# Kernel tuning notes

Hardware: AMD Instinct MI355X
Metric: run time of the kernel (lower is better)

Reference implementation:

```python
import jax, jax.numpy as jnp
import numpy as np

N_Q = 10000
B, S = 128, 200
M = 50          # memory_size
DK = 64         # memory_key_state_dim == q_embed_dim == final_fc_dim
DV = 128        # memory_value_state_dim == qa_embed_dim
F = 64          # final_fc_dim


def setup_inputs() -> dict:
    key = jax.random.key(0)
    ks = jax.random.split(key, 14)
    q_data = jax.random.randint(ks[0], (B, S), 0, N_Q + 1)
    qa_data = jax.random.randint(ks[1], (B, S), 0, 2 * N_Q + 1)
    # target in {-1 (pad), 0, 1}
    target = jax.random.randint(ks[2], (B, S), -1, 2).astype(jnp.float32)
    q_embed_w = jax.random.normal(ks[3], (N_Q + 1, DK), jnp.float32) * 0.1
    q_embed_w = q_embed_w.at[0].set(0.0)  # padding_idx=0
    qa_embed_w = jax.random.normal(ks[4], (2 * N_Q + 1, DV), jnp.float32) * 0.1
    qa_embed_w = qa_embed_w.at[0].set(0.0)
    mem_key = jax.random.normal(ks[5], (M, DK), jnp.float32) * (2.0 / DK) ** 0.5
    init_mem_value = jax.random.normal(ks[6], (M, DV), jnp.float32) * (2.0 / DV) ** 0.5
    erase_w = jax.random.normal(ks[7], (DV, DV), jnp.float32) * (2.0 / DV) ** 0.5
    erase_b = jnp.zeros((DV,), jnp.float32)
    add_w = jax.random.normal(ks[8], (DV, DV), jnp.float32) * (2.0 / DV) ** 0.5
    add_b = jnp.zeros((DV,), jnp.float32)
    read_w = jax.random.normal(ks[9], (F, DV + F), jnp.float32) * (2.0 / (DV + F)) ** 0.5
    read_b = jnp.zeros((F,), jnp.float32)
    pred_w = jax.random.normal(ks[10], (1, F), jnp.float32) * (2.0 / F) ** 0.5
    pred_b = jnp.zeros((1,), jnp.float32)
    return {
        'q_data': q_data, 'qa_data': qa_data, 'target': target,
        'q_embed_w': q_embed_w, 'qa_embed_w': qa_embed_w,
        'mem_key': mem_key, 'init_mem_value': init_mem_value,
        'erase_w': erase_w, 'erase_b': erase_b,
        'add_w': add_w, 'add_b': add_b,
        'read_w': read_w, 'read_b': read_b,
        'pred_w': pred_w, 'pred_b': pred_b,
    }


def reference(q_data, qa_data, target, q_embed_w, qa_embed_w, mem_key,
              init_mem_value, erase_w, erase_b, add_w, add_b,
              read_w, read_b, pred_w, pred_b):
    q_e = q_embed_w[q_data]    # [B,S,DK]
    qa_e = qa_embed_w[qa_data]  # [B,S,DV]
    Mv0 = jnp.broadcast_to(init_mem_value, (q_data.shape[0],) + init_mem_value.shape)  # [B,M,DV]

    def step(Mv, x):
        q, qa = x                                           # [B,DK], [B,DV]
        w = jax.nn.softmax(q @ mem_key.T, axis=1)           # addressing -> [B,M]
        read = jnp.einsum('bm,bmv->bv', w, Mv)              # weighted read (before write)
        e = jax.nn.sigmoid(qa @ erase_w.T + erase_b)        # [B,DV]
        a = jnp.tanh(qa @ add_w.T + add_b)                  # [B,DV]
        Mv_new = Mv * (1.0 - w[:, :, None] * e[:, None, :]) + w[:, :, None] * a[:, None, :]
        return Mv_new, read

    _, reads = jax.lax.scan(step, Mv0, (q_e.transpose(1, 0, 2), qa_e.transpose(1, 0, 2)))
    reads = reads.transpose(1, 0, 2)                        # [B,S,DV]

    h = jnp.tanh(jnp.concatenate([reads, q_e], axis=-1) @ read_w.T + read_b)  # [B,S,F]
    logits = (h @ pred_w.T + pred_b)[..., 0]                # [B,S]

    mask = target >= 0
    t = jnp.where(mask, target, 0.0)
    # stable BCE with logits
    bce = jnp.maximum(logits, 0.0) - logits * t + jnp.log1p(jnp.exp(-jnp.abs(logits)))
    n_valid = jnp.maximum(jnp.sum(mask.astype(jnp.float32)), 1.0)
    loss = jnp.sum(jnp.where(mask, bce, 0.0)) / n_valid
    probs = jnp.where(mask, jax.nn.sigmoid(logits), 0.0)    # masked predictions, fixed shape
    return loss, probs
```

## Files before the change

### kernel.cpp

```cpp
#include <hip/hip_runtime.h>
#include <math.h>

#define BB 128
#define SS 200
#define MM 50
#define DKK 64
#define DVV 128
#define FF 64
#define NROW (BB*SS)

#define WROW 64
#define NFCB (NROW/64)
#define WLDS 136
#define FLDS 200
#define CLEN 25
#define MP 25
#define NSCB 100

#define W_OFF   0L
#define EA_OFF  (W_OFF + (long)NROW*WROW)
#define R_OFF   (EA_OFF + (long)NROW*DVV*2)
#define ACC_OFF (R_OFF + (long)NROW*DVV)

typedef __attribute__((ext_vector_type(8))) short bf16x8;
typedef __attribute__((ext_vector_type(4))) float f32x4;
typedef __attribute__((ext_vector_type(2))) float f32x2;

__device__ __forceinline__ float rlane(float v, int l) {
    return __builtin_bit_cast(float, __builtin_amdgcn_readlane(__builtin_bit_cast(unsigned, v), l));
}
__device__ __forceinline__ short f2bf(float f) {
    unsigned u = __builtin_bit_cast(unsigned, f);
    u += 0x7fff + ((u >> 16) & 1);
    return (short)(u >> 16);
}
__device__ __forceinline__ bf16x8 cvt8(const float* p) {
    float4 lo = *(const float4*)p;
    float4 hi = *(const float4*)(p + 4);
    bf16x8 f;
    f[0] = f2bf(lo.x); f[1] = f2bf(lo.y); f[2] = f2bf(lo.z); f[3] = f2bf(lo.w);
    f[4] = f2bf(hi.x); f[5] = f2bf(hi.y); f[6] = f2bf(hi.z); f[7] = f2bf(hi.w);
    return f;
}

__global__ __launch_bounds__(256) void k_pre(const int* __restrict__ q_data,
                                             const float* __restrict__ q_embed_w,
                                             const float* __restrict__ mem_key,
                                             const int* __restrict__ qa_data,
                                             const float* __restrict__ qa_embed_w,
                                             const float* __restrict__ erase_w,
                                             const float* __restrict__ erase_b,
                                             const float* __restrict__ add_w,
                                             const float* __restrict__ add_b,
                                             float* __restrict__ w_out,
                                             float* __restrict__ EA,
                                             float* __restrict__ acc) {
    __shared__ union {
        short  wl[2 * 128 * WLDS];
        float4 mk[MM * 16];
    } sh;
    int tid = threadIdx.x;
    int bid = blockIdx.x;

    if (bid < NSCB) {
        if (bid == 0 && tid == 0) {
            acc[0] = 0.f; acc[1] = 0.f;
            ((unsigned*)acc)[2] = 0u;
        }
        const float4* mkg = (const float4*)mem_key;
        for (int i = tid; i < MM * 16; i += 256) sh.mk[i] = mkg[i];
        __syncthreads();

        int item = bid * 256 + tid;
        int qidx = q_data[item];
        const float4* qg = (const float4*)(q_embed_w + (long)qidx * DKK);
        float4 q[16];
#pragma unroll
        for (int i = 0; i < 16; i++) q[i] = qg[i];

        float s[MM];
        float mx = -1e30f;
#pragma unroll 2
        for (int m = 0; m < MM; m++) {
            float a = 0.f;
#pragma unroll
            for (int k4 = 0; k4 < 16; k4++) {
                float4 mkv = sh.mk[m * 16 + k4];
                float4 qv = q[k4];
                a = fmaf(qv.x, mkv.x, a);
                a = fmaf(qv.y, mkv.y, a);
                a = fmaf(qv.z, mkv.z, a);
                a = fmaf(qv.w, mkv.w, a);
            }
            s[m] = a;
            mx = fmaxf(mx, a);
        }
        float sum = 0.f;
#pragma unroll
        for (int m = 0; m < MM; m++) { s[m] = expf(s[m] - mx); sum += s[m]; }
        float inv = 1.f / sum;

        float* wo = w_out + (long)item * WROW;
#pragma unroll
        for (int m = 0; m < MM; m++) wo[m] = s[m] * inv;
#pragma unroll
        for (int m = MM; m < WROW; m++) wo[m] = 0.f;
        return;
    }

    int r0 = (bid - NSCB) * 64;
    int lane = tid & 63;
    int wv = tid >> 6;
    int n = lane & 15;
    int quad = lane >> 4;

    for (int i = tid; i < 8192; i += 256) {
        int mat = i >> 12;
        int r = (i >> 5) & 127;
        int p = i & 31;
        float4 src = *(const float4*)((mat ? add_w : erase_w) + r * 128 + p * 4);
        short4 d;
        d.x = f2bf(src.x); d.y = f2bf(src.y); d.z = f2bf(src.z); d.w = f2bf(src.w);
        *(short4*)(sh.wl + (mat * 128 + r) * WLDS + p * 4) = d;
    }

    int arow = r0 + wv * 16 + n;
    int qidx = qa_data[arow];
    const float* qp = qa_embed_w + (long)qidx * DVV + quad * 8;
    bf16x8 afrag[4];
#pragma unroll
    for (int kb = 0; kb < 4; kb++) afrag[kb] = cvt8(qp + kb * 32);

    float eb_[8], ab_[8];
#pragma unroll
    for (int vt = 0; vt < 8; vt++) {
        eb_[vt] = erase_b[vt * 16 + n];
        ab_[vt] = add_b[vt * 16 + n];
    }
    __syncthreads();

    int rowbase = r0 + wv * 16 + quad * 4;
#pragma unroll 2
    for (int vt = 0; vt < 8; vt++) {
        int vrow = vt * 16 + n;
        f32x4 ae = {0.f, 0.f, 0.f, 0.f};
        f32x4 aa = {0.f, 0.f, 0.f, 0.f};
#pragma unroll
        for (int kb = 0; kb < 4; kb++) {
            bf16x8 be = *(const bf16x8*)(sh.wl + vrow * WLDS + kb * 32 + quad * 8);
            bf16x8 ba = *(const bf16x8*)(sh.wl + (128 + vrow) * WLDS + kb * 32 + quad * 8);
            ae = __builtin_amdgcn_mfma_f32_16x16x32_bf16(afrag[kb], be, ae, 0, 0, 0);
            aa = __builtin_amdgcn_mfma_f32_16x16x32_bf16(afrag[kb], ba, aa, 0, 0, 0);
        }
        int v = vt * 16 + n;
        float eb = eb_[vt], ab = ab_[vt];
#pragma unroll
        for (int r = 0; r < 4; r++) {
            float ev = 1.f / (1.f + __expf(-(ae[r] + eb)));
            float av = 2.f / (1.f + __expf(-2.f * (aa[r] + ab))) - 1.f;
            float2 o; o.x = ev; o.y = av;
            *(float2*)(EA + (((long)(rowbase + r)) * DVV + v) * 2) = o;
        }
    }
}

__global__ __launch_bounds__(512, 2) void k_scan(const float* __restrict__ w_pad,
                                                 const float* __restrict__ EA,
                                                 const float* __restrict__ init_mv,
                                                 float* __restrict__ R) {
    __shared__ float Sb[MM * 64];
    int b   = blockIdx.x >> 1;
    int vh  = blockIdx.x & 1;
    int tid = threadIdx.x;
    int lane  = tid & 63;
    int chunk = tid >> 6;
    int v  = vh * 64 + lane;
    int t0 = chunk * CLEN;

    const float* wbase = w_pad + ((long)b * SS + t0) * WROW;
    const float* eab   = EA + (((long)b * SS + t0) * DVV + v) * 2;
    float*       Rb    = R + ((long)b * SS + t0) * DVV + v;

    const f32x2 one = {1.f, 1.f};

    f32x2 A2[MP], B2[MP];
#pragma unroll
    for (int j = 0; j < MP; j++) { A2[j] = one; B2[j] = (f32x2){0.f, 0.f}; }

    float  w_cur  = wbase[lane];
    float2 ea_cur = *(const float2*)eab;
#pragma unroll 1
    for (int t = 0; t < CLEN; t++) {
        int tp = (t + 1 < CLEN) ? t + 1 : t;
        float  w_nxt  = wbase[tp * WROW + lane];
        float2 ea_nxt = *(const float2*)(eab + (long)tp * DVV * 2);
        f32x2 e2 = {ea_cur.x, ea_cur.x};
        f32x2 a2 = {ea_cur.y, ea_cur.y};
#pragma unroll
        for (int j = 0; j < MP; j++) {
            f32x2 w2 = {rlane(w_cur, 2 * j), rlane(w_cur, 2 * j + 1)};
            f32x2 alpha = one - w2 * e2;
            A2[j] = A2[j] * alpha;
            B2[j] = alpha * B2[j] + w2 * a2;
        }
        w_cur = w_nxt; ea_cur = ea_nxt;
    }

    f32x2 Mv[MP];
    if (chunk == 0) {
#pragma unroll
        for (int j = 0; j < MP; j++) {
            Mv[j].x = init_mv[(2 * j) * DVV + v];
            Mv[j].y = init_mv[(2 * j + 1) * DVV + v];
        }
#pragma unroll
        for (int j = 0; j < MP; j++) {
            f32x2 nb = A2[j] * Mv[j] + B2[j];
            Sb[(2 * j) * 64 + lane] = nb.x;
            Sb[(2 * j + 1) * 64 + lane] = nb.y;
        }
    }
    __syncthreads();
    for (int c = 1; c < 8; c++) {
        if (chunk == c) {
#pragma unroll
            for (int j = 0; j < MP; j++) {
                Mv[j].x = Sb[(2 * j) * 64 + lane];
                Mv[j].y = Sb[(2 * j + 1) * 64 + lane];
            }
            if (c < 7) {
#pragma unroll
                for (int j = 0; j < MP; j++) {
                    f32x2 nb = A2[j] * Mv[j] + B2[j];
                    Sb[(2 * j) * 64 + lane] = nb.x;
                    Sb[(2 * j + 1) * 64 + lane] = nb.y;
                }
            }
        }
        __syncthreads();
    }

    w_cur  = wbase[lane];
    ea_cur = *(const float2*)eab;
#pragma unroll 1
    for (int t = 0; t < CLEN; t++) {
        int tp = (t + 1 < CLEN) ? t + 1 : t;
        float  w_nxt  = wbase[tp * WROW + lane];
        float2 ea_nxt = *(const float2*)(eab + (long)tp * DVV * 2);
        f32x2 e2 = {ea_cur.x, ea_cur.x};
        f32x2 a2 = {ea_cur.y, ea_cur.y};
        f32x2 rd2 = {0.f, 0.f};
#pragma unroll
        for (int j = 0; j < MP; j++) {
            f32x2 w2 = {rlane(w_cur, 2 * j), rlane(w_cur, 2 * j + 1)};
            rd2 = rd2 + w2 * Mv[j];
            f32x2 alpha = one - w2 * e2;
            Mv[j] = alpha * Mv[j] + w2 * a2;
        }
        Rb[t * DVV] = rd2.x + rd2.y;
        w_cur = w_nxt; ea_cur = ea_nxt;
    }
}

__global__ __launch_bounds__(256) void k_fc(const float* __restrict__ Rr,
                                            const int* __restrict__ q_data,
                                            const float* __restrict__ q_embed_w,
                                            const float* __restrict__ read_w,
                                            const float* __restrict__ read_b,
                                            const float* __restrict__ pred_w,
                                            const float* __restrict__ pred_b,
                                            const float* __restrict__ target,
                                            float* __restrict__ out,
                                            float* __restrict__ acc) {
    __shared__ short Wl[64 * FLDS];
    __shared__ float2 red[4];
    int tid = threadIdx.x;
    int r0 = blockIdx.x * 64;
    int lane = tid & 63;
    int wv = tid >> 6;
    int n = lane & 15;
    int quad = lane >> 4;

    for (int i = tid; i < 3072; i += 256) {
        int f = i / 48, p = i - f * 48;
        float4 src = *(const float4*)(read_w + f * 192 + p * 4);
        short4 d;
        d.x = f2bf(src.x); d.y = f2bf(src.y); d.z = f2bf(src.z); d.w = f2bf(src.w);
        *(short4*)(Wl + f * FLDS + p * 4) = d;
    }

    int arow = r0 + wv * 16 + n;
    const float* rp = Rr + (long)arow * DVV + quad * 8;
    int qi = q_data[arow];
    const float* qp = q_embed_w + (long)qi * DKK + quad * 8;
    bf16x8 afrag[6];
#pragma unroll
    for (int kb = 0; kb < 4; kb++) afrag[kb] = cvt8(rp + kb * 32);
#pragma unroll
    for (int kb = 0; kb < 2; kb++) afrag[4 + kb] = cvt8(qp + kb * 32);

    float rb_[4], pw_[4];
#pragma unroll
    for (int ft = 0; ft < 4; ft++) {
        rb_[ft] = read_b[ft * 16 + n];
        pw_[ft] = pred_w[ft * 16 + n];
    }
    float pb = pred_b[0];
    __syncthreads();

    int rowbase = r0 + wv * 16 + quad * 4;
    float pv[4] = {0.f, 0.f, 0.f, 0.f};
#pragma unroll
    for (int ft = 0; ft < 4; ft++) {
        int f = ft * 16 + n;
        f32x4 ac = {0.f, 0.f, 0.f, 0.f};
#pragma unroll
        for (int kb = 0; kb < 6; kb++) {
            bf16x8 bfr = *(const bf16x8*)(Wl + f * FLDS + kb * 32 + quad * 8);
            ac = __builtin_amdgcn_mfma_f32_16x16x32_bf16(afrag[kb], bfr, ac, 0, 0, 0);
        }
        float rb = rb_[ft], pw = pw_[ft];
#pragma unroll
        for (int r = 0; r < 4; r++) {
            float h = 2.f / (1.f + __expf(-2.f * (ac[r] + rb))) - 1.f;
            pv[r] = fmaf(pw, h, pv[r]);
        }
    }

    float bce_sum = 0.f, cnt = 0.f;
#pragma unroll
    for (int r = 0; r < 4; r++) {
        float p = pv[r];
        p += __shfl_xor(p, 1, 64);
        p += __shfl_xor(p, 2, 64);
        p += __shfl_xor(p, 4, 64);
        p += __shfl_xor(p, 8, 64);
        if (n == 0) {
            int row = rowbase + r;
            float tgt = target[row];
            float logit = p + pb;
            float prob = 0.f;
            if (tgt >= 0.f) {
                prob = 1.f / (1.f + __expf(-logit));
                float bce = fmaxf(logit, 0.f) - logit * tgt + log1pf(__expf(-fabsf(logit)));
                bce_sum += bce;
                cnt += 1.f;
            }
            out[1 + row] = prob;
        }
    }
    bce_sum += __shfl_xor(bce_sum, 16, 64);
    bce_sum += __shfl_xor(bce_sum, 32, 64);
    cnt     += __shfl_xor(cnt, 16, 64);
    cnt     += __shfl_xor(cnt, 32, 64);
    if (lane == 0) { red[wv].x = bce_sum; red[wv].y = cnt; }
    __syncthreads();
    if (tid == 0) {
        float bsum = red[0].x + red[1].x + red[2].x + red[3].x;
        float csum = red[0].y + red[1].y + red[2].y + red[3].y;
        atomicAdd(&acc[0], bsum);
        atomicAdd(&acc[1], csum);
        __threadfence();
        unsigned prev = atomicAdd((unsigned*)acc + 2, 1u);
        if (prev == NFCB - 1) {
            __threadfence();
            float B = atomicAdd(&acc[0], 0.f);
            float C = atomicAdd(&acc[1], 0.f);
            out[0] = B / fmaxf(C, 1.f);
        }
    }
}

extern "C" void kernel_launch(void* const* d_in, const int* in_sizes, int n_in,
                              void* d_out, int out_size, void* d_ws, size_t ws_size,
                              hipStream_t stream) {
    const int*   q_data     = (const int*)d_in[0];
    const int*   qa_data    = (const int*)d_in[1];
    const float* target     = (const float*)d_in[2];
    const float* q_embed_w  = (const float*)d_in[3];
    const float* qa_embed_w = (const float*)d_in[4];
    const float* mem_key    = (const float*)d_in[5];
    const float* init_mv    = (const float*)d_in[6];
    const float* erase_w    = (const float*)d_in[7];
    const float* erase_b    = (const float*)d_in[8];
    const float* add_w      = (const float*)d_in[9];
    const float* add_b      = (const float*)d_in[10];
    const float* read_w     = (const float*)d_in[11];
    const float* read_b     = (const float*)d_in[12];
    const float* pred_w     = (const float*)d_in[13];
    const float* pred_b     = (const float*)d_in[14];
    float* out = (float*)d_out;
    float* ws  = (float*)d_ws;

    float* w_all = ws + W_OFF;
    float* EA    = ws + EA_OFF;
    float* R     = ws + R_OFF;
    float* acc   = ws + ACC_OFF;

    k_pre<<<NSCB + NROW / 64, 256, 0, stream>>>(q_data, q_embed_w, mem_key,
                                                qa_data, qa_embed_w,
                                                erase_w, erase_b, add_w, add_b,
                                                w_all, EA, acc);
    k_scan<<<BB * 2, 512, 0, stream>>>(w_all, EA, init_mv, R);
    k_fc<<<NFCB, 256, 0, stream>>>(R, q_data, q_embed_w, read_w, read_b,
                                   pred_w, pred_b, target, out, acc);
}
```

Measured before the change: 182.2 us.

## Split scan memory slots across two blocks and sum partial reads in FC

The recurrent scan kernel now splits the 50 memory slots into two halves handled by separate blocks, doubling the grid to 512 blocks and halving the serial per-thread work and register state. Each half writes its own partial read vector, and the FC kernel adds the two partials before converting to bf16. This trades extra global writes and reads of a second read buffer for more parallelism on the latency-bound scan. Padded slots beyond 50 rely on zero addressing weights in the padded w buffer.

```diff
diff --git a/kernel.cpp b/kernel.cpp
--- a/kernel.cpp
+++ b/kernel.cpp
@@ -14,13 +14,14 @@
 #define WLDS 136
 #define FLDS 200
 #define CLEN 25
-#define MP 25
+#define MPH 13
 #define NSCB 100
 
 #define W_OFF   0L
 #define EA_OFF  (W_OFF + (long)NROW*WROW)
 #define R_OFF   (EA_OFF + (long)NROW*DVV*2)
-#define ACC_OFF (R_OFF + (long)NROW*DVV)
+#define RP1_OFF (R_OFF + (long)NROW*DVV)
+#define ACC_OFF (RP1_OFF + (long)NROW*DVV)
 
 typedef __attribute__((ext_vector_type(8))) short bf16x8;
 typedef __attribute__((ext_vector_type(4))) float f32x4;
@@ -40,6 +41,16 @@
     bf16x8 f;
     f[0] = f2bf(lo.x); f[1] = f2bf(lo.y); f[2] = f2bf(lo.z); f[3] = f2bf(lo.w);
     f[4] = f2bf(hi.x); f[5] = f2bf(hi.y); f[6] = f2bf(hi.z); f[7] = f2bf(hi.w);
+    return f;
+}
+__device__ __forceinline__ bf16x8 cvt8sum(const float* p, const float* q) {
+    float4 alo = *(const float4*)p, ahi = *(const float4*)(p + 4);
+    float4 blo = *(const float4*)q, bhi = *(const float4*)(q + 4);
+    bf16x8 f;
+    f[0] = f2bf(alo.x + blo.x); f[1] = f2bf(alo.y + blo.y);
+    f[2] = f2bf(alo.z + blo.z); f[3] = f2bf(alo.w + blo.w);
+    f[4] = f2bf(ahi.x + bhi.x); f[5] = f2bf(ahi.y + bhi.y);
+    f[6] = f2bf(ahi.z + bhi.z); f[7] = f2bf(ahi.w + bhi.w);
     return f;
 }
 
@@ -167,25 +178,31 @@
 __global__ __launch_bounds__(512, 2) void k_scan(const float* __restrict__ w_pad,
                                                  const float* __restrict__ EA,
                                                  const float* __restrict__ init_mv,
-                                                 float* __restrict__ R) {
-    __shared__ float Sb[MM * 64];
-    int b   = blockIdx.x >> 1;
-    int vh  = blockIdx.x & 1;
+                                                 float* __restrict__ Rp0,
+                                                 float* __restrict__ Rp1) {
+    __shared__ float Sb[52 * 64];
+    int bid = blockIdx.x;
+    int mh  = bid & 1;
+    int vh  = (bid >> 1) & 1;
+    int b   = bid >> 2;
     int tid = threadIdx.x;
     int lane  = tid & 63;
     int chunk = tid >> 6;
     int v  = vh * 64 + lane;
     int t0 = chunk * CLEN;
+    int j0 = mh * MPH;
+    int l0 = 2 * j0;
+    int sb0 = l0 * 64 + lane;
 
     const float* wbase = w_pad + ((long)b * SS + t0) * WROW;
     const float* eab   = EA + (((long)b * SS + t0) * DVV + v) * 2;
-    float*       Rb    = R + ((long)b * SS + t0) * DVV + v;
+    float*       Rb    = (mh ? Rp1 : Rp0) + ((long)b * SS + t0) * DVV + v;
 
     const f32x2 one = {1.f, 1.f};
 
-    f32x2 A2[MP], B2[MP];
-#pragma unroll
-    for (int j = 0; j < MP; j++) { A2[j] = one; B2[j] = (f32x2){0.f, 0.f}; }
+    f32x2 A2[MPH], B2[MPH];
+#pragma unroll
+    for (int j = 0; j < MPH; j++) { A2[j] = one; B2[j] = (f32x2){0.f, 0.f}; }
 
     float  w_cur  = wbase[lane];
     float2 ea_cur = *(const float2*)eab;
@@ -197,8 +214,8 @@
         f32x2 e2 = {ea_cur.x, ea_cur.x};
         f32x2 a2 = {ea_cur.y, ea_cur.y};
 #pragma unroll
-        for (int j = 0; j < MP; j++) {
-            f32x2 w2 = {rlane(w_cur, 2 * j), rlane(w_cur, 2 * j + 1)};
+        for (int j = 0; j < MPH; j++) {
+            f32x2 w2 = {rlane(w_cur, l0 + 2 * j), rlane(w_cur, l0 + 2 * j + 1)};
             f32x2 alpha = one - w2 * e2;
             A2[j] = A2[j] * alpha;
             B2[j] = alpha * B2[j] + w2 * a2;
@@ -206,34 +223,37 @@
         w_cur = w_nxt; ea_cur = ea_nxt;
     }
 
-    f32x2 Mv[MP];
+    f32x2 Mv[MPH];
     if (chunk == 0) {
 #pragma unroll
-        for (int j = 0; j < MP; j++) {
-            Mv[j].x = init_mv[(2 * j) * DVV + v];
-            Mv[j].y = init_mv[(2 * j + 1) * DVV + v];
-        }
-#pragma unroll
-        for (int j = 0; j < MP; j++) {
+        for (int j = 0; j < MPH; j++) {
+            int m0 = l0 + 2 * j, m1 = m0 + 1;
+            if (m0 > MM - 2) m0 = MM - 2;
+            if (m1 > MM - 1) m1 = MM - 1;
+            Mv[j].x = init_mv[m0 * DVV + v];
+            Mv[j].y = init_mv[m1 * DVV + v];
+        }
+#pragma unroll
+        for (int j = 0; j < MPH; j++) {
             f32x2 nb = A2[j] * Mv[j] + B2[j];
-            Sb[(2 * j) * 64 + lane] = nb.x;
-            Sb[(2 * j + 1) * 64 + lane] = nb.y;
+            Sb[sb0 + (2 * j) * 64] = nb.x;
+            Sb[sb0 + (2 * j + 1) * 64] = nb.y;
         }
     }
     __syncthreads();
     for (int c = 1; c < 8; c++) {
         if (chunk == c) {
 #pragma unroll
-            for (int j = 0; j < MP; j++) {
-                Mv[j].x = Sb[(2 * j) * 64 + lane];
-                Mv[j].y = Sb[(2 * j + 1) * 64 + lane];
+            for (int j = 0; j < MPH; j++) {
+                Mv[j].x = Sb[sb0 + (2 * j) * 64];
+                Mv[j].y = Sb[sb0 + (2 * j + 1) * 64];
             }
             if (c < 7) {
 #pragma unroll
-                for (int j = 0; j < MP; j++) {
+                for (int j = 0; j < MPH; j++) {
                     f32x2 nb = A2[j] * Mv[j] + B2[j];
-                    Sb[(2 * j) * 64 + lane] = nb.x;
-                    Sb[(2 * j + 1) * 64 + lane] = nb.y;
+                    Sb[sb0 + (2 * j) * 64] = nb.x;
+                    Sb[sb0 + (2 * j + 1) * 64] = nb.y;
                 }
             }
         }
@@ -251,8 +271,8 @@
         f32x2 a2 = {ea_cur.y, ea_cur.y};
         f32x2 rd2 = {0.f, 0.f};
 #pragma unroll
-        for (int j = 0; j < MP; j++) {
-            f32x2 w2 = {rlane(w_cur, 2 * j), rlane(w_cur, 2 * j + 1)};
+        for (int j = 0; j < MPH; j++) {
+            f32x2 w2 = {rlane(w_cur, l0 + 2 * j), rlane(w_cur, l0 + 2 * j + 1)};
             rd2 = rd2 + w2 * Mv[j];
             f32x2 alpha = one - w2 * e2;
             Mv[j] = alpha * Mv[j] + w2 * a2;
@@ -262,7 +282,8 @@
     }
 }
 
-__global__ __launch_bounds__(256) void k_fc(const float* __restrict__ Rr,
+__global__ __launch_bounds__(256) void k_fc(const float* __restrict__ Rp0,
+                                            const float* __restrict__ Rp1,
                                             const int* __restrict__ q_data,
                                             const float* __restrict__ q_embed_w,
                                             const float* __restrict__ read_w,
@@ -290,12 +311,13 @@
     }
 
     int arow = r0 + wv * 16 + n;
-    const float* rp = Rr + (long)arow * DVV + quad * 8;
+    const float* rp0 = Rp0 + (long)arow * DVV + quad * 8;
+    const float* rp1 = Rp1 + (long)arow * DVV + quad * 8;
     int qi = q_data[arow];
     const float* qp = q_embed_w + (long)qi * DKK + quad * 8;
     bf16x8 afrag[6];
 #pragma unroll
-    for (int kb = 0; kb < 4; kb++) afrag[kb] = cvt8(rp + kb * 32);
+    for (int kb = 0; kb < 4; kb++) afrag[kb] = cvt8sum(rp0 + kb * 32, rp1 + kb * 32);
 #pragma unroll
     for (int kb = 0; kb < 2; kb++) afrag[4 + kb] = cvt8(qp + kb * 32);
 
@@ -394,14 +416,15 @@
 
     float* w_all = ws + W_OFF;
     float* EA    = ws + EA_OFF;
-    float* R     = ws + R_OFF;
+    float* Rp0   = ws + R_OFF;
+    float* Rp1   = ws + RP1_OFF;
     float* acc   = ws + ACC_OFF;
 
     k_pre<<<NSCB + NROW / 64, 256, 0, stream>>>(q_data, q_embed_w, mem_key,
                                                 qa_data, qa_embed_w,
                                                 erase_w, erase_b, add_w, add_b,
                                                 w_all, EA, acc);
-    k_scan<<<BB * 2, 512, 0, stream>>>(w_all, EA, init_mv, R);
-    k_fc<<<NFCB, 256, 0, stream>>>(R, q_data, q_embed_w, read_w, read_b,
+    k_scan<<<BB * 4, 512, 0, stream>>>(w_all, EA, init_mv, Rp0, Rp1);
+    k_fc<<<NFCB, 256, 0, stream>>>(Rp0, Rp1, q_data, q_embed_w, read_w, read_b,
                                    pred_w, pred_b, target, out, acc);
 }
```

Result: slower. 193.6 us (+6.3%).

## Stage addressing weights in LDS and skip redundant scan passes

Applied to the files above, without the earlier changes.

The scan kernel now copies the whole per-batch softmax weight row block into shared memory and reads weights as broadcast float4 LDS loads instead of readlane from a per-lane global load. Chunk 0 runs the read pass directly from the initial memory instead of computing an unused affine summary, and chunk 7 skips pass 1 since its summary is never consumed. The update is refactored into FMA-friendly form (Mv + w*(a - e*Mv)) with deeper EA prefetch. It costs 51KB of LDS per block and drops to one block per CU via launch bounds, which reduces occupancy.

```diff
diff --git a/kernel.cpp b/kernel.cpp
--- a/kernel.cpp
+++ b/kernel.cpp
@@ -26,9 +26,6 @@
 typedef __attribute__((ext_vector_type(4))) float f32x4;
 typedef __attribute__((ext_vector_type(2))) float f32x2;
 
-__device__ __forceinline__ float rlane(float v, int l) {
-    return __builtin_bit_cast(float, __builtin_amdgcn_readlane(__builtin_bit_cast(unsigned, v), l));
-}
 __device__ __forceinline__ short f2bf(float f) {
     unsigned u = __builtin_bit_cast(unsigned, f);
     u += 0x7fff + ((u >> 16) & 1);
@@ -164,10 +161,81 @@
     }
 }
 
-__global__ __launch_bounds__(512, 2) void k_scan(const float* __restrict__ w_pad,
+__device__ __forceinline__ void scan_pass1(const float4* __restrict__ wq,
+                                           const float* __restrict__ eab,
+                                           f32x2* A2, f32x2* B2) {
+    const f32x2 one = {1.f, 1.f};
+    float2 e0 = *(const float2*)eab;
+    float2 e1 = *(const float2*)(eab + (long)1 * DVV * 2);
+#pragma unroll 1
+    for (int t = 0; t < CLEN; t++) {
+        int tp = (t + 2 < CLEN) ? t + 2 : CLEN - 1;
+        float2 en = *(const float2*)(eab + (long)tp * DVV * 2);
+        f32x2 ne2 = {-e0.x, -e0.x};
+        f32x2 a2  = {e0.y, e0.y};
+#pragma unroll
+        for (int c = 0; c < 13; c++) {
+            float4 q = wq[t * 16 + c];
+            {
+                int j = 2 * c;
+                f32x2 w2 = {q.x, q.y};
+                f32x2 al = w2 * ne2 + one;
+                A2[j] = A2[j] * al;
+                B2[j] = al * B2[j] + w2 * a2;
+            }
+            if (c < 12) {
+                int j = 2 * c + 1;
+                f32x2 w2 = {q.z, q.w};
+                f32x2 al = w2 * ne2 + one;
+                A2[j] = A2[j] * al;
+                B2[j] = al * B2[j] + w2 * a2;
+            }
+        }
+        e0 = e1; e1 = en;
+    }
+}
+
+__device__ __forceinline__ void scan_pass2(const float4* __restrict__ wq,
+                                           const float* __restrict__ eab,
+                                           float* __restrict__ Rb,
+                                           f32x2* Mv) {
+    float2 e0 = *(const float2*)eab;
+    float2 e1 = *(const float2*)(eab + (long)1 * DVV * 2);
+#pragma unroll 1
+    for (int t = 0; t < CLEN; t++) {
+        int tp = (t + 2 < CLEN) ? t + 2 : CLEN - 1;
+        float2 en = *(const float2*)(eab + (long)tp * DVV * 2);
+        f32x2 ne2 = {-e0.x, -e0.x};
+        f32x2 a2  = {e0.y, e0.y};
+        f32x2 rd  = {0.f, 0.f};
+#pragma unroll
+        for (int c = 0; c < 13; c++) {
+            float4 q = wq[t * 16 + c];
+            {
+                int j = 2 * c;
+                f32x2 w2 = {q.x, q.y};
+                rd = rd + w2 * Mv[j];
+                f32x2 s = ne2 * Mv[j] + a2;
+                Mv[j] = Mv[j] + w2 * s;
+            }
+            if (c < 12) {
+                int j = 2 * c + 1;
+                f32x2 w2 = {q.z, q.w};
+                rd = rd + w2 * Mv[j];
+                f32x2 s = ne2 * Mv[j] + a2;
+                Mv[j] = Mv[j] + w2 * s;
+            }
+        }
+        Rb[t * DVV] = rd.x + rd.y;
+        e0 = e1; e1 = en;
+    }
+}
+
+__global__ __launch_bounds__(512, 1) void k_scan(const float* __restrict__ w_pad,
                                                  const float* __restrict__ EA,
                                                  const float* __restrict__ init_mv,
                                                  float* __restrict__ R) {
+    __shared__ float Wl[SS * WROW];
     __shared__ float Sb[MM * 64];
     int b   = blockIdx.x >> 1;
     int vh  = blockIdx.x & 1;
@@ -177,50 +245,40 @@
     int v  = vh * 64 + lane;
     int t0 = chunk * CLEN;
 
-    const float* wbase = w_pad + ((long)b * SS + t0) * WROW;
-    const float* eab   = EA + (((long)b * SS + t0) * DVV + v) * 2;
-    float*       Rb    = R + ((long)b * SS + t0) * DVV + v;
+    {
+        const float4* wg = (const float4*)(w_pad + (long)b * SS * WROW);
+        float4* wl4 = (float4*)Wl;
+        for (int i = tid; i < SS * WROW / 4; i += 512) wl4[i] = wg[i];
+    }
+    __syncthreads();
+
+    const float4* wq  = (const float4*)(Wl + t0 * WROW);
+    const float*  eab = EA + (((long)b * SS + t0) * DVV + v) * 2;
+    float*        Rb  = R + ((long)b * SS + t0) * DVV + v;
 
     const f32x2 one = {1.f, 1.f};
-
     f32x2 A2[MP], B2[MP];
-#pragma unroll
-    for (int j = 0; j < MP; j++) { A2[j] = one; B2[j] = (f32x2){0.f, 0.f}; }
-
-    float  w_cur  = wbase[lane];
-    float2 ea_cur = *(const float2*)eab;
-#pragma unroll 1
-    for (int t = 0; t < CLEN; t++) {
-        int tp = (t + 1 < CLEN) ? t + 1 : t;
-        float  w_nxt  = wbase[tp * WROW + lane];
-        float2 ea_nxt = *(const float2*)(eab + (long)tp * DVV * 2);
-        f32x2 e2 = {ea_cur.x, ea_cur.x};
-        f32x2 a2 = {ea_cur.y, ea_cur.y};
-#pragma unroll
-        for (int j = 0; j < MP; j++) {
-            f32x2 w2 = {rlane(w_cur, 2 * j), rlane(w_cur, 2 * j + 1)};
-            f32x2 alpha = one - w2 * e2;
-            A2[j] = A2[j] * alpha;
-            B2[j] = alpha * B2[j] + w2 * a2;
-        }
-        w_cur = w_nxt; ea_cur = ea_nxt;
-    }
-
     f32x2 Mv[MP];
+
     if (chunk == 0) {
 #pragma unroll
         for (int j = 0; j < MP; j++) {
             Mv[j].x = init_mv[(2 * j) * DVV + v];
             Mv[j].y = init_mv[(2 * j + 1) * DVV + v];
         }
+        scan_pass2(wq, eab, Rb, Mv);
 #pragma unroll
         for (int j = 0; j < MP; j++) {
-            f32x2 nb = A2[j] * Mv[j] + B2[j];
-            Sb[(2 * j) * 64 + lane] = nb.x;
-            Sb[(2 * j + 1) * 64 + lane] = nb.y;
-        }
+            Sb[(2 * j) * 64 + lane] = Mv[j].x;
+            Sb[(2 * j + 1) * 64 + lane] = Mv[j].y;
+        }
+    } else if (chunk < 7) {
+#pragma unroll
+        for (int j = 0; j < MP; j++) { A2[j] = one; B2[j] = (f32x2){0.f, 0.f}; }
+        scan_pass1(wq, eab, A2, B2);
     }
     __syncthreads();
+
     for (int c = 1; c < 8; c++) {
         if (chunk == c) {
 #pragma unroll
@@ -240,26 +298,7 @@
         __syncthreads();
     }
 
-    w_cur  = wbase[lane];
-    ea_cur = *(const float2*)eab;
-#pragma unroll 1
-    for (int t = 0; t < CLEN; t++) {
-        int tp = (t + 1 < CLEN) ? t + 1 : t;
-        float  w_nxt  = wbase[tp * WROW + lane];
-        float2 ea_nxt = *(const float2*)(eab + (long)tp * DVV * 2);
-        f32x2 e2 = {ea_cur.x, ea_cur.x};
-        f32x2 a2 = {ea_cur.y, ea_cur.y};
-        f32x2 rd2 = {0.f, 0.f};
-#pragma unroll
-        for (int j = 0; j < MP; j++) {
-            f32x2 w2 = {rlane(w_cur, 2 * j), rlane(w_cur, 2 * j + 1)};
-            rd2 = rd2 + w2 * Mv[j];
-            f32x2 alpha = one - w2 * e2;
-            Mv[j] = alpha * Mv[j] + w2 * a2;
-        }
-        Rb[t * DVV] = rd2.x + rd2.y;
-        w_cur = w_nxt; ea_cur = ea_nxt;
-    }
+    if (chunk > 0) scan_pass2(wq, eab, Rb, Mv);
 }
 
 __global__ __launch_bounds__(256) void k_fc(const float* __restrict__ Rr,
```

Result: no change. 183.0 us (+0.4%).
